# Optimization experiments

Hardware: AMD Instinct MI355X
Metric: run time of the kernel (lower is better)

Reference implementation:

```python
import jax, jax.numpy as jnp
import numpy as np

CHUNK = 64  # batch chunk so the [chunk, n, n] intermediate stays ~1 GB

def setup_inputs() -> dict:
    key = jax.random.key(0)
    k1, k2 = jax.random.split(key)
    B, n = 256, 2048
    x = jax.random.normal(k1, (B, n), dtype=jnp.float32)
    M = jax.random.normal(k2, (n, n), dtype=jnp.float32)
    return {"x": x, "M": M}

def reference(x, M):
    # Tropical (max-times) matvec: out[b, i] = max_j M[i, j] * x[b, j]
    B, n = x.shape
    xc = x.reshape(B // CHUNK, CHUNK, n)
    def per_chunk(xb):  # xb: [CHUNK, n]
        # [CHUNK, n, n] intermediate, reduced with max over j
        return jnp.max(M[None, :, :] * xb[:, None, :], axis=2)
    out = jax.lax.map(per_chunk, xc)  # [B//CHUNK, CHUNK, n]
    return out.reshape(B, n)
```

## Files before the change

kernel.cpp:

```cpp
#include <hip/hip_runtime.h>

static constexpr int N_DIM = 2048;
static constexpr int BB = 64;
static constexpr int BI = 128;
static constexpr int BJ = 32;
static constexpr int UB = 4;
static constexpr int VI = 8;
static constexpr int XP = 36;

typedef float f32x2 __attribute__((ext_vector_type(2)));

template<int JSPLIT>
__global__ __launch_bounds__(256, 4)
void tropical_main(const float* __restrict__ x, const float* __restrict__ M,
                   float* __restrict__ dst, int B)
{
    constexpr int JRANGE = N_DIM / JSPLIT;
    constexpr int NCH = JRANGE / BJ;

    __shared__ float xs[BB][XP];
    __shared__ float Ms[BI][XP];

    const int t  = threadIdx.x;
    const int bt = t & 15;
    const int it = t >> 4;

    const int perjs  = gridDim.x / JSPLIT;
    const int js     = blockIdx.x / perjs;
    const int rem    = blockIdx.x % perjs;
    const int itiles = N_DIM / BI;
    const int b0 = (rem / itiles) * BB;
    const int i0 = (rem % itiles) * BI;
    const int jb = js * JRANGE;

    float acc[UB][VI];
#pragma unroll
    for (int u = 0; u < UB; ++u)
#pragma unroll
        for (int v = 0; v < VI; ++v)
            acc[u][v] = -__builtin_inff();

#pragma unroll 1
    for (int ch = 0; ch < NCH; ++ch) {
        const int j0 = jb + ch * BJ;
        __syncthreads();
#pragma unroll
        for (int q = 0; q < 2; ++q) {
            const int idx = q * 256 + t;
            const int r = idx >> 3, c = idx & 7;
            const float4 v = *(const float4*)(x + (size_t)(b0 + r) * N_DIM + j0 + c * 4);
            *(float4*)&xs[r][c * 4] = v;
        }
#pragma unroll
        for (int q = 0; q < 4; ++q) {
            const int idx = q * 256 + t;
            const int r = idx >> 3, c = idx & 7;
            const float4 v = *(const float4*)(M + (size_t)(i0 + r) * N_DIM + j0 + c * 4);
            *(float4*)&Ms[r][(c ^ ((r >> 3) & 7)) * 4] = v;
        }
        __syncthreads();

#pragma unroll
        for (int jg = 0; jg < BJ / 4; ++jg) {
            float4 xv[UB];
#pragma unroll
            for (int u = 0; u < UB; ++u)
                xv[u] = *(const float4*)&xs[bt + 16 * u][jg * 4];
            const int mc = (jg ^ (it & 7)) * 4;
#pragma unroll
            for (int v = 0; v < VI; ++v) {
                const float4 mv = *(const float4*)&Ms[it * 8 + v][mc];
                const f32x2 ml = {mv.x, mv.y}, mh = {mv.z, mv.w};
#pragma unroll
                for (int u = 0; u < UB; ++u) {
                    const f32x2 xl = {xv[u].x, xv[u].y}, xh = {xv[u].z, xv[u].w};
                    const f32x2 pl = ml * xl;
                    const f32x2 ph = mh * xh;
                    float a = acc[u][v];
                    a = fmaxf(fmaxf(a, pl.x), pl.y);
                    a = fmaxf(fmaxf(a, ph.x), ph.y);
                    acc[u][v] = a;
                }
            }
        }
    }

#pragma unroll
    for (int u = 0; u < UB; ++u) {
        float* o = dst + ((size_t)js * B + b0 + bt + 16 * u) * N_DIM + i0 + it * 8;
        *(float4*)o       = make_float4(acc[u][0], acc[u][1], acc[u][2], acc[u][3]);
        *(float4*)(o + 4) = make_float4(acc[u][4], acc[u][5], acc[u][6], acc[u][7]);
    }
}

template<int JSPLIT>
__global__ __launch_bounds__(256)
void tropical_comb(const float* __restrict__ part, float* __restrict__ out, int total4)
{
    const int idx = blockIdx.x * 256 + threadIdx.x;
    if (idx >= total4) return;
    const float4* p = (const float4*)part;
    float4 a = p[idx];
#pragma unroll
    for (int s = 1; s < JSPLIT; ++s) {
        const float4 v = p[idx + (size_t)s * total4];
        a.x = fmaxf(a.x, v.x); a.y = fmaxf(a.y, v.y);
        a.z = fmaxf(a.z, v.z); a.w = fmaxf(a.w, v.w);
    }
    ((float4*)out)[idx] = a;
}

extern "C" void kernel_launch(void* const* d_in, const int* in_sizes, int n_in,
                              void* d_out, int out_size, void* d_ws, size_t ws_size,
                              hipStream_t stream)
{
    const float* x = (const float*)d_in[0];
    const float* M = (const float*)d_in[1];
    float* out = (float*)d_out;

    const int B = in_sizes[0] / N_DIM;
    const int base = (B / BB) * (N_DIM / BI);
    const size_t slab = (size_t)B * N_DIM * sizeof(float);
    const int total4 = B * N_DIM / 4;
    const int cblocks = (total4 + 255) / 256;

#define RUN_JS(JS)                                                                      \
    do {                                                                                \
        float* dst = (JS == 1) ? out : (float*)d_ws;                                    \
        hipLaunchKernelGGL(tropical_main<JS>, dim3(base * JS), dim3(256), 0, stream,    \
                           x, M, dst, B);                                               \
        if (JS > 1)                                                                     \
            hipLaunchKernelGGL(tropical_comb<JS>, dim3(cblocks), dim3(256), 0, stream,  \
                               (const float*)d_ws, out, total4);                        \
    } while (0)

    if      (ws_size >= 16 * slab) RUN_JS(16);
    else if (ws_size >=  8 * slab) RUN_JS(8);
    else if (ws_size >=  4 * slab) RUN_JS(4);
    else if (ws_size >=  2 * slab) RUN_JS(2);
    else                           RUN_JS(1);
#undef RUN_JS
}
```

Baseline: 113.4 us.

## Enlarge tropical matvec tile to 128x128 with double-buffered register-staged prefetch

Grows the per-block output tile from 64x128 to 128x128, so each thread accumulates 8x8 outputs instead of 4x8 and reuses every loaded shared value twice as often. It adds double-buffered shared memory, with the global loads for chunk c+2 held in registers while chunk c is computed, so only one barrier is needed per chunk. The inner loop uses inline v_pk_mul_f32 and v_max3_f32 assembly to cut VALU instruction count. In exchange, register pressure rises (launch bounds drop from 4 to 2 blocks per SM), there are half as many blocks, and the JS=1 and JS=2 fallbacks are removed, so the code always needs enough workspace for at least four split slabs.

Result: no change. 112.6 us (-0.7%).

```diff
diff --git a/kernel.cpp b/kernel.cpp
--- a/kernel.cpp
+++ b/kernel.cpp
@@ -1,108 +1,147 @@
 #include <hip/hip_runtime.h>
 
+typedef float f32x2 __attribute__((ext_vector_type(2)));
+typedef float f32x4 __attribute__((ext_vector_type(4)));
+
 static constexpr int N_DIM = 2048;
-static constexpr int BB = 64;
-static constexpr int BI = 128;
 static constexpr int BJ = 32;
-static constexpr int UB = 4;
-static constexpr int VI = 8;
-static constexpr int XP = 36;
 
-typedef float f32x2 __attribute__((ext_vector_type(2)));
+__device__ __forceinline__ float vmax3(float a, float b, float c) {
+    float d;
+    asm("v_max3_f32 %0, %1, %2, %3" : "=v"(d) : "v"(a), "v"(b), "v"(c));
+    return d;
+}
+__device__ __forceinline__ f32x2 pkmul(f32x2 a, f32x2 b) {
+    f32x2 d;
+    asm("v_pk_mul_f32 %0, %1, %2" : "=v"(d) : "v"(a), "v"(b));
+    return d;
+}
 
-template<int JSPLIT>
-__global__ __launch_bounds__(256, 4)
-void tropical_main(const float* __restrict__ x, const float* __restrict__ M,
-                   float* __restrict__ dst, int B)
+template<int JS>
+__global__ __launch_bounds__(256, 2)
+void trop_main(const float* __restrict__ x, const float* __restrict__ M,
+               float* __restrict__ dst, int B)
 {
-    constexpr int JRANGE = N_DIM / JSPLIT;
+    constexpr int JRANGE = N_DIM / JS;
     constexpr int NCH = JRANGE / BJ;
 
-    __shared__ float xs[BB][XP];
-    __shared__ float Ms[BI][XP];
+    __shared__ f32x4 xsh[2][128][8];
+    __shared__ f32x4 msh[2][128][8];
 
     const int t  = threadIdx.x;
     const int bt = t & 15;
     const int it = t >> 4;
 
-    const int perjs  = gridDim.x / JSPLIT;
-    const int js     = blockIdx.x / perjs;
-    const int rem    = blockIdx.x % perjs;
-    const int itiles = N_DIM / BI;
-    const int b0 = (rem / itiles) * BB;
-    const int i0 = (rem % itiles) * BI;
-    const int jb = js * JRANGE;
+    const int bid = blockIdx.x;
+    const int bpj = (B >> 7) << 4;
+    const int js  = bid / bpj;
+    const int rem = bid - js * bpj;
+    const int g     = rem >> 4;
+    const int itile = rem & 15;
 
-    float acc[UB][VI];
+    const int b0 = g * 128;
+    const int i0 = itile * 128;
+    const int jseg = js * JRANGE;
+
+    const int sr = t >> 3;
+    const int sc = t & 7;
+    const float* xg[4]; const float* mg[4];
+    int xq[4], mq[4];
 #pragma unroll
-    for (int u = 0; u < UB; ++u)
+    for (int p = 0; p < 4; ++p) {
+        const int r = 32 * p + sr;
+        xg[p] = x + (size_t)(b0 + r) * N_DIM + jseg + sc * 4;
+        mg[p] = M + (size_t)(i0 + r) * N_DIM + jseg + sc * 4;
+        xq[p] = sc ^ (r & 7);
+        mq[p] = sc ^ ((r >> 3) & 7);
+    }
+
+    f32x4 pxv[4], pmv[4];
+    auto ldchunk = [&](int ch) {
+        const int off = ch * BJ;
 #pragma unroll
-        for (int v = 0; v < VI; ++v)
+        for (int p = 0; p < 4; ++p) {
+            pxv[p] = *(const f32x4*)(xg[p] + off);
+            pmv[p] = *(const f32x4*)(mg[p] + off);
+        }
+    };
+    auto wrchunk = [&](int s) {
+#pragma unroll
+        for (int p = 0; p < 4; ++p) {
+            xsh[s][32 * p + sr][xq[p]] = pxv[p];
+            msh[s][32 * p + sr][mq[p]] = pmv[p];
+        }
+    };
+
+    float acc[8][8];
+#pragma unroll
+    for (int u = 0; u < 8; ++u)
+#pragma unroll
+        for (int v = 0; v < 8; ++v)
             acc[u][v] = -__builtin_inff();
 
+    ldchunk(0);
+    wrchunk(0);
+    if (NCH > 1) ldchunk(1);
+    __syncthreads();
+
 #pragma unroll 1
-    for (int ch = 0; ch < NCH; ++ch) {
-        const int j0 = jb + ch * BJ;
-        __syncthreads();
-#pragma unroll
-        for (int q = 0; q < 2; ++q) {
-            const int idx = q * 256 + t;
-            const int r = idx >> 3, c = idx & 7;
-            const float4 v = *(const float4*)(x + (size_t)(b0 + r) * N_DIM + j0 + c * 4);
-            *(float4*)&xs[r][c * 4] = v;
+    for (int c = 0; c < NCH; ++c) {
+        const int cur = c & 1;
+
+        if (c + 1 < NCH) {
+            wrchunk(cur ^ 1);
+            if (c + 2 < NCH) ldchunk(c + 2);
         }
-#pragma unroll
-        for (int q = 0; q < 4; ++q) {
-            const int idx = q * 256 + t;
-            const int r = idx >> 3, c = idx & 7;
-            const float4 v = *(const float4*)(M + (size_t)(i0 + r) * N_DIM + j0 + c * 4);
-            *(float4*)&Ms[r][(c ^ ((r >> 3) & 7)) * 4] = v;
-        }
-        __syncthreads();
 
 #pragma unroll
-        for (int jg = 0; jg < BJ / 4; ++jg) {
-            float4 xv[UB];
+        for (int jg = 0; jg < 8; ++jg) {
+            f32x4 xv[8], mv[8];
 #pragma unroll
-            for (int u = 0; u < UB; ++u)
-                xv[u] = *(const float4*)&xs[bt + 16 * u][jg * 4];
-            const int mc = (jg ^ (it & 7)) * 4;
+            for (int u = 0; u < 8; ++u)
+                xv[u] = xsh[cur][bt + 16 * u][jg ^ (bt & 7)];
 #pragma unroll
-            for (int v = 0; v < VI; ++v) {
-                const float4 mv = *(const float4*)&Ms[it * 8 + v][mc];
-                const f32x2 ml = {mv.x, mv.y}, mh = {mv.z, mv.w};
+            for (int v = 0; v < 8; ++v)
+                mv[v] = msh[cur][it * 8 + v][jg ^ (it & 7)];
 #pragma unroll
-                for (int u = 0; u < UB; ++u) {
-                    const f32x2 xl = {xv[u].x, xv[u].y}, xh = {xv[u].z, xv[u].w};
-                    const f32x2 pl = ml * xl;
-                    const f32x2 ph = mh * xh;
+            for (int v = 0; v < 8; ++v) {
+                const f32x2 ml = __builtin_shufflevector(mv[v], mv[v], 0, 1);
+                const f32x2 mh = __builtin_shufflevector(mv[v], mv[v], 2, 3);
+#pragma unroll
+                for (int u = 0; u < 8; ++u) {
+                    const f32x2 xl = __builtin_shufflevector(xv[u], xv[u], 0, 1);
+                    const f32x2 xh = __builtin_shufflevector(xv[u], xv[u], 2, 3);
+                    const f32x2 p0 = pkmul(xl, ml);
+                    const f32x2 p1 = pkmul(xh, mh);
                     float a = acc[u][v];
-                    a = fmaxf(fmaxf(a, pl.x), pl.y);
-                    a = fmaxf(fmaxf(a, ph.x), ph.y);
+                    a = vmax3(a, p0.x, p0.y);
+                    a = vmax3(a, p1.x, p1.y);
                     acc[u][v] = a;
                 }
             }
         }
+        __syncthreads();
     }
 
+    float* dw = dst + ((size_t)js * B + b0 + bt) * N_DIM + i0 + it * 8;
 #pragma unroll
-    for (int u = 0; u < UB; ++u) {
-        float* o = dst + ((size_t)js * B + b0 + bt + 16 * u) * N_DIM + i0 + it * 8;
-        *(float4*)o       = make_float4(acc[u][0], acc[u][1], acc[u][2], acc[u][3]);
-        *(float4*)(o + 4) = make_float4(acc[u][4], acc[u][5], acc[u][6], acc[u][7]);
+    for (int u = 0; u < 8; ++u) {
+        float* row = dw + (size_t)(16 * u) * N_DIM;
+        *(float4*)row       = make_float4(acc[u][0], acc[u][1], acc[u][2], acc[u][3]);
+        *(float4*)(row + 4) = make_float4(acc[u][4], acc[u][5], acc[u][6], acc[u][7]);
     }
 }
 
-template<int JSPLIT>
+template<int JS>
 __global__ __launch_bounds__(256)
-void tropical_comb(const float* __restrict__ part, float* __restrict__ out, int total4)
+void trop_comb(const float* __restrict__ part, float* __restrict__ out, int total4)
 {
     const int idx = blockIdx.x * 256 + threadIdx.x;
     if (idx >= total4) return;
     const float4* p = (const float4*)part;
     float4 a = p[idx];
 #pragma unroll
-    for (int s = 1; s < JSPLIT; ++s) {
+    for (int s = 1; s < JS; ++s) {
         const float4 v = p[idx + (size_t)s * total4];
         a.x = fmaxf(a.x, v.x); a.y = fmaxf(a.y, v.y);
         a.z = fmaxf(a.z, v.z); a.w = fmaxf(a.w, v.w);
@@ -119,25 +158,21 @@
     float* out = (float*)d_out;
 
     const int B = in_sizes[0] / N_DIM;
-    const int base = (B / BB) * (N_DIM / BI);
+    const int bpj = (B >> 7) << 4;
     const size_t slab = (size_t)B * N_DIM * sizeof(float);
     const int total4 = B * N_DIM / 4;
     const int cblocks = (total4 + 255) / 256;
 
-#define RUN_JS(JS)                                                                      \
+#define RUN_JS(JSV)                                                                     \
     do {                                                                                \
-        float* dst = (JS == 1) ? out : (float*)d_ws;                                    \
-        hipLaunchKernelGGL(tropical_main<JS>, dim3(base * JS), dim3(256), 0, stream,    \
-                           x, M, dst, B);                                               \
-        if (JS > 1)                                                                     \
-            hipLaunchKernelGGL(tropical_comb<JS>, dim3(cblocks), dim3(256), 0, stream,  \
-                               (const float*)d_ws, out, total4);                        \
+        hipLaunchKernelGGL(trop_main<JSV>, dim3(bpj * JSV), dim3(256), 0, stream,       \
+                           x, M, (float*)d_ws, B);                                      \
+        hipLaunchKernelGGL(trop_comb<JSV>, dim3(cblocks), dim3(256), 0, stream,         \
+                           (const float*)d_ws, out, total4);                            \
     } while (0)
 
     if      (ws_size >= 16 * slab) RUN_JS(16);
     else if (ws_size >=  8 * slab) RUN_JS(8);
-    else if (ws_size >=  4 * slab) RUN_JS(4);
-    else if (ws_size >=  2 * slab) RUN_JS(2);
-    else                           RUN_JS(1);
+    else                           RUN_JS(4);
 #undef RUN_JS
 }
```
